# Optimization experiments

Measured on AMD Instinct MI355X. Metric: run time of the kernel, lower is better.

The kernel has to match this reference:

```python
import jax, jax.numpy as jnp
import numpy as np

B, T, N, E = 8, 32, 128, 2048
IN_DIM, HID, OUT = 512, 512, 512
SLOPE = 0.2  # GATConv default negative_slope


def setup_inputs() -> dict:
    key = jax.random.key(0)
    ks = jax.random.split(key, 12)
    x = jax.random.normal(ks[0], (B, T, N, IN_DIM), jnp.float32)
    edge_index = jax.random.randint(ks[1], (B, T, 2, E), 0, N)
    valid_step_index = jax.random.randint(ks[2], (B,), 1, T + 1)
    def lin(k, o, i):
        return jax.random.normal(k, (o, i), jnp.float32) / np.sqrt(i).astype(np.float32)
    W1 = lin(ks[3], HID, IN_DIM)
    a1_src = jax.random.normal(ks[4], (HID,), jnp.float32) / np.sqrt(HID).astype(np.float32)
    a1_dst = jax.random.normal(ks[5], (HID,), jnp.float32) / np.sqrt(HID).astype(np.float32)
    b1 = jnp.zeros((HID,), jnp.float32)
    W2 = lin(ks[6], OUT, HID)
    a2_src = jax.random.normal(ks[7], (OUT,), jnp.float32) / np.sqrt(OUT).astype(np.float32)
    a2_dst = jax.random.normal(ks[8], (OUT,), jnp.float32) / np.sqrt(OUT).astype(np.float32)
    b2 = jnp.zeros((OUT,), jnp.float32)
    W_time = jax.random.normal(ks[9], (T, T), jnp.float32) / np.sqrt(T).astype(np.float32)
    b_time = jnp.zeros((T,), jnp.float32)
    return dict(x=x, edge_index=edge_index, valid_step_index=valid_step_index,
                W1=W1, a1_src=a1_src, a1_dst=a1_dst, b1=b1,
                W2=W2, a2_src=a2_src, a2_dst=a2_dst, b2=b2,
                W_time=W_time, b_time=b_time)


def _gat(x, src, dst, W, a_src, a_dst, b):
    # Single-head PyG GATConv (concat=True, heads=1), self-loops already appended.
    n = x.shape[0]
    h = x @ W.T                                             # [N, H]
    e = jax.nn.leaky_relu((h @ a_src)[src] + (h @ a_dst)[dst], SLOPE)  # [E]
    m = jax.ops.segment_max(e, dst, num_segments=n)
    m = jnp.where(jnp.isfinite(m), m, 0.0)
    p = jnp.exp(e - m[dst])
    denom = jax.ops.segment_sum(p, dst, num_segments=n)
    alpha = p / denom[dst]                                  # segment softmax over incoming edges
    return jax.ops.segment_sum(h[src] * alpha[:, None], dst, num_segments=n) + b


def reference(x, edge_index, valid_step_index, W1, a1_src, a1_dst, b1,
              W2, a2_src, a2_dst, b2, W_time, b_time):
    b_, t_, n_, _ = x.shape
    g = b_ * t_
    xf = x.reshape(g, n_, -1)
    ei = edge_index.reshape(g, 2, -1)
    # add self loops (PyG GATConv default add_self_loops=True)
    loops = jnp.broadcast_to(jnp.arange(n_)[None, None, :], (g, 2, n_))
    ei = jnp.concatenate([ei, loops], axis=-1)
    src, dst = ei[:, 0], ei[:, 1]
    gat = jax.vmap(_gat, in_axes=(0, 0, 0, None, None, None, None))
    h = jax.nn.gelu(gat(xf, src, dst, W1, a1_src, a1_dst, b1), approximate=False)
    # F.dropout(p=0.2) is identity in eval mode
    h = gat(h, src, dst, W2, a2_src, a2_dst, b2)
    y = h.reshape(b_, t_, n_, -1)
    mask = (jnp.arange(t_)[None, :] < valid_step_index[:, None]).astype(y.dtype)
    y = y * mask[:, :, None, None]
    # TemporalConv: Conv2d(T, T, 1) over time-as-channel = linear mix across time, then GELU, residual
    fused = jax.nn.gelu(jnp.einsum('ts,bsnf->btnf', W_time, y)
                        + b_time[None, :, None, None], approximate=False)
    return fused + y
```

## Files before the change

### kernel.cpp

```cpp
#include <hip/hip_runtime.h>

using u16 = unsigned short;
using u32 = unsigned int;

typedef __bf16 bf16x8 __attribute__((ext_vector_type(8)));
typedef float  f32x4  __attribute__((ext_vector_type(4)));

__device__ __forceinline__ u16 f2bf(float f) {
    u32 u = __float_as_uint(f);
    u32 r = u + 0x7fffu + ((u >> 16) & 1u);
    return (u16)(r >> 16);
}
__device__ __forceinline__ float gelu_f(float x) {
    return 0.5f * x * (1.0f + erff(x * 0.70710678118654752440f));
}

#define GLOAD16(gp, lp) __builtin_amdgcn_global_load_lds( \
    (const __attribute__((address_space(1))) void*)(gp),  \
    (__attribute__((address_space(3))) void*)(lp), 16, 0, 0)

__global__ __launch_bounds__(256) void prep_kernel(
    const float* __restrict__ x, const float* __restrict__ W1, const float* __restrict__ W2,
    u16* __restrict__ Xb, u16* __restrict__ W1b, u16* __restrict__ W2b,
    float* __restrict__ Z)
{
    const int i0 = blockIdx.x * 256 + threadIdx.x;
    const int stride = gridDim.x * 256;
    if (i0 < 32768) ((float4*)Z)[i0] = make_float4(0.f, 0.f, 0.f, 0.f);
    for (int i = i0; i < 65536; i += stride) {
        float4 v = ((const float4*)W1)[i];
        ushort4 o; o.x = f2bf(v.x); o.y = f2bf(v.y); o.z = f2bf(v.z); o.w = f2bf(v.w);
        ((ushort4*)W1b)[i] = o;
    }
    for (int i = i0; i < 65536; i += stride) {
        float4 v = ((const float4*)W2)[i];
        ushort4 o; o.x = f2bf(v.x); o.y = f2bf(v.y); o.z = f2bf(v.z); o.w = f2bf(v.w);
        ((ushort4*)W2b)[i] = o;
    }
    for (int i = i0; i < 4194304; i += stride) {
        float4 v = ((const float4*)x)[i];
        ushort4 o; o.x = f2bf(v.x); o.y = f2bf(v.y); o.z = f2bf(v.z); o.w = f2bf(v.w);
        ((ushort4*)Xb)[i] = o;
    }
}

__global__ __launch_bounds__(256) void gat_gemm(
    const u16* __restrict__ A, const u16* __restrict__ Wb,
    const float* __restrict__ a_s, const float* __restrict__ a_d,
    u16* __restrict__ HT, float* __restrict__ SS, float* __restrict__ SD)
{
    __shared__ __align__(16) u16 As[128 * 32];
    __shared__ __align__(16) u16 Bs[128 * 32];
    __shared__ float sA[128], dA[128];

    const int tid  = threadIdx.x;
    const int lane = tid & 63;
    const int w    = tid >> 6;
    const int wm   = w & 1, wn = w >> 1;
    const int fr   = lane & 15;
    const int grp  = lane >> 4;
    const int ko   = grp * 8;
    const int g    = blockIdx.x >> 2;
    const int tn   = (blockIdx.x & 3) * 128;

    if (tid < 128) { sA[tid] = 0.f; dA[tid] = 0.f; }

    const int srow = lane >> 2;
    const int skel = (lane & 3) * 8;
    const u16* Ag0 = A  + (size_t)g * 65536 + (size_t)(w * 32 + srow) * 512 + skel;
    const u16* Bg0 = Wb + (size_t)(tn + w * 32 + srow) * 512 + skel;
    u16* Asl = &As[w * 1024];
    u16* Bsl = &Bs[w * 1024];

    f32x4 acc[4][4] = {};

    for (int kt = 0; kt < 16; ++kt) {
        GLOAD16(Ag0 + kt * 32,            Asl);
        GLOAD16(Ag0 + 16 * 512 + kt * 32, Asl + 512);
        GLOAD16(Bg0 + kt * 32,            Bsl);
        GLOAD16(Bg0 + 16 * 512 + kt * 32, Bsl + 512);
        __syncthreads();
        bf16x8 af[4], bf[4];
        #pragma unroll
        for (int i = 0; i < 4; ++i) {
            af[i] = *(const bf16x8*)&As[(wm * 64 + i * 16 + fr) * 32 + ko];
            bf[i] = *(const bf16x8*)&Bs[(wn * 64 + i * 16 + fr) * 32 + ko];
        }
        #pragma unroll
        for (int i = 0; i < 4; ++i)
            #pragma unroll
            for (int j = 0; j < 4; ++j)
                acc[i][j] = __builtin_amdgcn_mfma_f32_16x16x32_bf16(af[i], bf[j], acc[i][j], 0, 0, 0);
        __syncthreads();
    }

    float asv[4], adv[4];
    #pragma unroll
    for (int j = 0; j < 4; ++j) {
        int f = tn + wn * 64 + j * 16 + fr;
        asv[j] = a_s[f]; adv[j] = a_d[f];
    }
    u16* Hg = HT + (size_t)g * 65536;
    #pragma unroll
    for (int i = 0; i < 4; ++i) {
        int node0 = wm * 64 + i * 16 + grp * 4;
        #pragma unroll
        for (int j = 0; j < 4; ++j) {
            int f = tn + wn * 64 + j * 16 + fr;
            ushort4 o;
            o.x = f2bf(acc[i][j][0]); o.y = f2bf(acc[i][j][1]);
            o.z = f2bf(acc[i][j][2]); o.w = f2bf(acc[i][j][3]);
            *(ushort4*)&Hg[(size_t)f * 128 + node0] = o;
        }
        #pragma unroll
        for (int r = 0; r < 4; ++r) {
            float s = acc[i][0][r] * asv[0] + acc[i][1][r] * asv[1]
                    + acc[i][2][r] * asv[2] + acc[i][3][r] * asv[3];
            float d = acc[i][0][r] * adv[0] + acc[i][1][r] * adv[1]
                    + acc[i][2][r] * adv[2] + acc[i][3][r] * adv[3];
            #pragma unroll
            for (int off = 1; off < 16; off <<= 1) {
                s += __shfl_xor(s, off);
                d += __shfl_xor(d, off);
            }
            if (fr == 0) {
                atomicAdd(&sA[node0 + r], s);
                atomicAdd(&dA[node0 + r], d);
            }
        }
    }
    __syncthreads();
    if (tid < 128) {
        atomicAdd(&SS[g * 128 + tid], sA[tid]);
        atomicAdd(&SD[g * 128 + tid], dA[tid]);
    }
}

template<int MODE>
__global__ __launch_bounds__(512) void gat_agg(
    const u16* __restrict__ HT, const int* __restrict__ ei,
    const float* __restrict__ SS, const float* __restrict__ SD,
    const float* __restrict__ bias, const int* __restrict__ valid,
    u16* __restrict__ outU, float* __restrict__ outF)
{
    __shared__ u16 Hts[65536];
    __shared__ u32 cntw[2048];
    __shared__ float stf[512];

    const int tid  = threadIdx.x;
    const int lane = tid & 63;
    const int w    = tid >> 6;
    const int rl   = lane & 15;
    const int grp  = lane >> 4;
    const int g    = blockIdx.x;
    const int bb   = g >> 5, tt = g & 31;

    const int4* es = (const int4*)(ei + (size_t)g * 4096);
    int4 e0 = es[tid], e1 = es[512 + tid];

    const u16* Hg = HT + (size_t)g * 65536;
    #pragma unroll
    for (int it = 0; it < 16; ++it) {
        int f = it * 32 + (tid >> 4);
        int blk = tid & 15;
        GLOAD16(Hg + (size_t)f * 128 + ((blk ^ (f & 15)) * 8), &Hts[it * 4096 + w * 512]);
    }

    for (int i = tid; i < 2048; i += 512) cntw[i] = 0u;
    if (tid < 128) {
        stf[tid]       = SS[g * 128 + tid];
        stf[128 + tid] = SD[g * 128 + tid];
    }
    __syncthreads();

    atomicAdd(&cntw[e1.x * 16 + (e0.x >> 3)], 1u << ((e0.x & 7) * 4));
    atomicAdd(&cntw[e1.y * 16 + (e0.y >> 3)], 1u << ((e0.y & 7) * 4));
    atomicAdd(&cntw[e1.z * 16 + (e0.z >> 3)], 1u << ((e0.z & 7) * 4));
    atomicAdd(&cntw[e1.w * 16 + (e0.w >> 3)], 1u << ((e0.w & 7) * 4));
    if (tid < 128) atomicAdd(&cntw[tid * 16 + (tid >> 3)], 1u << ((tid & 7) * 4));
    __syncthreads();

    for (int r = 0; r < 16; ++r) {
        int m = w * 16 + r;
        float sdm = stf[128 + m];
        u32 w0 = cntw[m * 16 + (lane >> 3)];
        u32 w1 = cntw[m * 16 + 8 + (lane >> 3)];
        u32 c0 = (w0 >> ((lane & 7) * 4)) & 15u;
        u32 c1 = (w1 >> ((lane & 7) * 4)) & 15u;
        float E0 = stf[lane] + sdm;      E0 = E0 > 0.f ? E0 : 0.2f * E0;
        float E1 = stf[lane + 64] + sdm; E1 = E1 > 0.f ? E1 : 0.2f * E1;
        float mx = fmaxf(c0 ? E0 : -1e30f, c1 ? E1 : -1e30f);
        #pragma unroll
        for (int off = 1; off < 64; off <<= 1) mx = fmaxf(mx, __shfl_xor(mx, off));
        float p = (c0 ? (float)c0 * __expf(E0 - mx) : 0.f)
                + (c1 ? (float)c1 * __expf(E1 - mx) : 0.f);
        #pragma unroll
        for (int off = 1; off < 64; off <<= 1) p += __shfl_xor(p, off);
        if (lane == 0) { stf[256 + m] = mx; stf[384 + m] = 1.f / p; }
    }
    __syncthreads();

    const int m = w * 16 + rl;
    const float sdm = stf[128 + m], Mm = stf[256 + m], rDm = stf[384 + m];
    bf16x8 pa[4];
    #pragma unroll
    for (int kb = 0; kb < 4; ++kb) {
        u32 word = cntw[m * 16 + kb * 4 + grp];
        #pragma unroll
        for (int e = 0; e < 8; ++e) {
            u32 c = (word >> (e * 4)) & 15u;
            int s = kb * 32 + grp * 8 + e;
            float ev = stf[s] + sdm; ev = ev > 0.f ? ev : 0.2f * ev;
            float p = c ? (float)c * __expf(ev - Mm) * rDm : 0.f;
            pa[kb][e] = (__bf16)p;
        }
    }

    const float msk = (MODE == 1) ? ((tt < valid[bb]) ? 1.f : 0.f) : 1.f;
    #pragma unroll 1
    for (int jc = 0; jc < 8; ++jc) {
        f32x4 acc2[4] = {};
        #pragma unroll
        for (int j4 = 0; j4 < 4; ++j4) {
            int f = jc * 64 + j4 * 16 + rl;
            #pragma unroll
            for (int kb = 0; kb < 4; ++kb) {
                bf16x8 hb = *(const bf16x8*)&Hts[f * 128 + (((kb * 4 + grp) ^ (f & 15)) * 8)];
                acc2[j4] = __builtin_amdgcn_mfma_f32_16x16x32_bf16(pa[kb], hb, acc2[j4], 0, 0, 0);
            }
        }
        #pragma unroll
        for (int j4 = 0; j4 < 4; ++j4) {
            int f = jc * 64 + j4 * 16 + rl;
            float bv = bias[f];
            #pragma unroll
            for (int r = 0; r < 4; ++r) {
                int m2 = w * 16 + grp * 4 + r;
                if (MODE == 0)
                    outU[(size_t)g * 65536 + m2 * 512 + f] = f2bf(gelu_f(acc2[j4][r] + bv));
                else
                    outF[(size_t)g * 65536 + m2 * 512 + f] = (acc2[j4][r] + bv) * msk;
            }
        }
    }
}

__global__ __launch_bounds__(256) void timemix_kernel(float* __restrict__ y,
                                                      const float* __restrict__ Wt,
                                                      const float* __restrict__ bt) {
    __shared__ float wsm[1024];
    __shared__ float bts[32];
    int tid = threadIdx.x;
    for (int i = tid; i < 1024; i += 256) wsm[i] = Wt[i];
    if (tid < 32) bts[tid] = bt[tid];
    __syncthreads();
    int blk = blockIdx.x;
    int b = blk >> 8;
    int rem = blk & 255;
    int n = rem >> 1;
    int f = (rem & 1) * 256 + tid;
    size_t base = ((size_t)b * 4096 + n) * 512 + f;
    float ys[32];
    #pragma unroll
    for (int s = 0; s < 32; ++s) ys[s] = y[base + (size_t)s * 65536];
    #pragma unroll
    for (int t = 0; t < 32; ++t) {
        float a = bts[t];
        #pragma unroll
        for (int s = 0; s < 32; ++s) a += wsm[t * 32 + s] * ys[s];
        y[base + (size_t)t * 65536] = gelu_f(a) + ys[t];
    }
}

extern "C" void kernel_launch(void* const* d_in, const int* in_sizes, int n_in,
                              void* d_out, int out_size, void* d_ws, size_t ws_size,
                              hipStream_t stream) {
    const float* x     = (const float*)d_in[0];
    const int*   ei    = (const int*)d_in[1];
    const int*   valid = (const int*)d_in[2];
    const float* W1    = (const float*)d_in[3];
    const float* a1s   = (const float*)d_in[4];
    const float* a1d   = (const float*)d_in[5];
    const float* b1    = (const float*)d_in[6];
    const float* W2    = (const float*)d_in[7];
    const float* a2s   = (const float*)d_in[8];
    const float* a2d   = (const float*)d_in[9];
    const float* b2    = (const float*)d_in[10];
    const float* Wt    = (const float*)d_in[11];
    const float* bt    = (const float*)d_in[12];
    float* out = (float*)d_out;

    char* ws = (char*)d_ws;
    u16* Xb    = (u16*)(ws);
    u16* HTb   = (u16*)(ws + 33554432);
    u16* W1b   = (u16*)(ws + 67108864);
    u16* W2b   = (u16*)(ws + 67633152);
    float* SS1 = (float*)(ws + 68157440);
    float* SD1 = (float*)(ws + 68288512);
    float* SS2 = (float*)(ws + 68419584);
    float* SD2 = (float*)(ws + 68550656);

    prep_kernel<<<2048, 256, 0, stream>>>(x, W1, W2, Xb, W1b, W2b, SS1);

    gat_gemm<<<1024, 256, 0, stream>>>(Xb, W1b, a1s, a1d, HTb, SS1, SD1);
    gat_agg<0><<<256, 512, 0, stream>>>(HTb, ei, SS1, SD1, b1, nullptr, Xb, nullptr);

    gat_gemm<<<1024, 256, 0, stream>>>(Xb, W2b, a2s, a2d, HTb, SS2, SD2);
    gat_agg<1><<<256, 512, 0, stream>>>(HTb, ei, SS2, SD2, b2, valid, nullptr, out);

    timemix_kernel<<<2048, 256, 0, stream>>>(out, Wt, bt);
}
```

Measured before the change: 194.8 us.

## Double-buffer GEMM LDS tiles, remap blocks per XCD, split aggregation across halves

The GEMM kernel now double-buffers its A/B LDS tiles, prefetching the next k-tile while MFMAs run on the current one. Block IDs are remapped so neighbouring graphs land on the same XCD. The aggregation kernel no longer stages the whole 128KB H tile in LDS. Instead each graph is split across two blocks by feature half, and H is read directly from global memory. This cuts LDS use and doubles the block count. The cost is that each half redundantly recomputes edge counts and the softmax, and H fragments now come from L2 instead of LDS.

Measured after the change: 214.6 us. 1.1x slower.

```diff
diff --git a/kernel.cpp b/kernel.cpp
--- a/kernel.cpp
+++ b/kernel.cpp
@@ -49,8 +49,8 @@
     const float* __restrict__ a_s, const float* __restrict__ a_d,
     u16* __restrict__ HT, float* __restrict__ SS, float* __restrict__ SD)
 {
-    __shared__ __align__(16) u16 As[128 * 32];
-    __shared__ __align__(16) u16 Bs[128 * 32];
+    __shared__ __align__(16) u16 As[2][128 * 32];
+    __shared__ __align__(16) u16 Bs[2][128 * 32];
     __shared__ float sA[128], dA[128];
 
     const int tid  = threadIdx.x;
@@ -60,8 +60,9 @@
     const int fr   = lane & 15;
     const int grp  = lane >> 4;
     const int ko   = grp * 8;
-    const int g    = blockIdx.x >> 2;
-    const int tn   = (blockIdx.x & 3) * 128;
+    const int bid  = (blockIdx.x & 7) * 128 + (blockIdx.x >> 3);
+    const int g    = bid >> 2;
+    const int tn   = (bid & 3) * 128;
 
     if (tid < 128) { sA[tid] = 0.f; dA[tid] = 0.f; }
 
@@ -69,22 +70,29 @@
     const int skel = (lane & 3) * 8;
     const u16* Ag0 = A  + (size_t)g * 65536 + (size_t)(w * 32 + srow) * 512 + skel;
     const u16* Bg0 = Wb + (size_t)(tn + w * 32 + srow) * 512 + skel;
-    u16* Asl = &As[w * 1024];
-    u16* Bsl = &Bs[w * 1024];
 
     f32x4 acc[4][4] = {};
 
+    GLOAD16(Ag0,            &As[0][w * 1024]);
+    GLOAD16(Ag0 + 16 * 512, &As[0][w * 1024 + 512]);
+    GLOAD16(Bg0,            &Bs[0][w * 1024]);
+    GLOAD16(Bg0 + 16 * 512, &Bs[0][w * 1024 + 512]);
+    __syncthreads();
+
     for (int kt = 0; kt < 16; ++kt) {
-        GLOAD16(Ag0 + kt * 32,            Asl);
-        GLOAD16(Ag0 + 16 * 512 + kt * 32, Asl + 512);
-        GLOAD16(Bg0 + kt * 32,            Bsl);
-        GLOAD16(Bg0 + 16 * 512 + kt * 32, Bsl + 512);
-        __syncthreads();
+        const int cur = kt & 1;
+        if (kt < 15) {
+            const int nb = cur ^ 1;
+            GLOAD16(Ag0 + (kt + 1) * 32,            &As[nb][w * 1024]);
+            GLOAD16(Ag0 + 16 * 512 + (kt + 1) * 32, &As[nb][w * 1024 + 512]);
+            GLOAD16(Bg0 + (kt + 1) * 32,            &Bs[nb][w * 1024]);
+            GLOAD16(Bg0 + 16 * 512 + (kt + 1) * 32, &Bs[nb][w * 1024 + 512]);
+        }
         bf16x8 af[4], bf[4];
         #pragma unroll
         for (int i = 0; i < 4; ++i) {
-            af[i] = *(const bf16x8*)&As[(wm * 64 + i * 16 + fr) * 32 + ko];
-            bf[i] = *(const bf16x8*)&Bs[(wn * 64 + i * 16 + fr) * 32 + ko];
+            af[i] = *(const bf16x8*)&As[cur][(wm * 64 + i * 16 + fr) * 32 + ko];
+            bf[i] = *(const bf16x8*)&Bs[cur][(wn * 64 + i * 16 + fr) * 32 + ko];
         }
         #pragma unroll
         for (int i = 0; i < 4; ++i)
@@ -143,7 +151,6 @@
     const float* __restrict__ bias, const int* __restrict__ valid,
     u16* __restrict__ outU, float* __restrict__ outF)
 {
-    __shared__ u16 Hts[65536];
     __shared__ u32 cntw[2048];
     __shared__ float stf[512];
 
@@ -152,19 +159,13 @@
     const int w    = tid >> 6;
     const int rl   = lane & 15;
     const int grp  = lane >> 4;
-    const int g    = blockIdx.x;
+    const int q    = blockIdx.x;
+    const int g    = (q & 7) * 32 + (q >> 4);
+    const int hf   = (q >> 3) & 1;
     const int bb   = g >> 5, tt = g & 31;
 
     const int4* es = (const int4*)(ei + (size_t)g * 4096);
     int4 e0 = es[tid], e1 = es[512 + tid];
-
-    const u16* Hg = HT + (size_t)g * 65536;
-    #pragma unroll
-    for (int it = 0; it < 16; ++it) {
-        int f = it * 32 + (tid >> 4);
-        int blk = tid & 15;
-        GLOAD16(Hg + (size_t)f * 128 + ((blk ^ (f & 15)) * 8), &Hts[it * 4096 + w * 512]);
-    }
 
     for (int i = tid; i < 2048; i += 512) cntw[i] = 0u;
     if (tid < 128) {
@@ -216,16 +217,17 @@
         }
     }
 
+    const u16* Hg = HT + (size_t)g * 65536;
     const float msk = (MODE == 1) ? ((tt < valid[bb]) ? 1.f : 0.f) : 1.f;
     #pragma unroll 1
-    for (int jc = 0; jc < 8; ++jc) {
+    for (int jc = hf * 4; jc < hf * 4 + 4; ++jc) {
         f32x4 acc2[4] = {};
         #pragma unroll
         for (int j4 = 0; j4 < 4; ++j4) {
             int f = jc * 64 + j4 * 16 + rl;
             #pragma unroll
             for (int kb = 0; kb < 4; ++kb) {
-                bf16x8 hb = *(const bf16x8*)&Hts[f * 128 + (((kb * 4 + grp) ^ (f & 15)) * 8)];
+                bf16x8 hb = *(const bf16x8*)&Hg[(size_t)f * 128 + (kb * 4 + grp) * 8];
                 acc2[j4] = __builtin_amdgcn_mfma_f32_16x16x32_bf16(pa[kb], hb, acc2[j4], 0, 0, 0);
             }
         }
@@ -303,10 +305,10 @@
     prep_kernel<<<2048, 256, 0, stream>>>(x, W1, W2, Xb, W1b, W2b, SS1);
 
     gat_gemm<<<1024, 256, 0, stream>>>(Xb, W1b, a1s, a1d, HTb, SS1, SD1);
-    gat_agg<0><<<256, 512, 0, stream>>>(HTb, ei, SS1, SD1, b1, nullptr, Xb, nullptr);
+    gat_agg<0><<<512, 512, 0, stream>>>(HTb, ei, SS1, SD1, b1, nullptr, Xb, nullptr);
 
     gat_gemm<<<1024, 256, 0, stream>>>(Xb, W2b, a2s, a2d, HTb, SS2, SD2);
-    gat_agg<1><<<256, 512, 0, stream>>>(HTb, ei, SS2, SD2, b2, valid, nullptr, out);
+    gat_agg<1><<<512, 512, 0, stream>>>(HTb, ei, SS2, SD2, b2, valid, nullptr, out);
 
     timemix_kernel<<<2048, 256, 0, stream>>>(out, Wt, bt);
 }
```
